# Kernel optimization log

Measured on AMD Instinct MI355X. Metric: run time of the kernel, lower is better.

The kernel has to match this reference:

```python
import jax, jax.numpy as jnp
import numpy as np

D_MODEL = 1024
H = 16
D_K = D_MODEL // H


def setup_inputs() -> dict:
    key = jax.random.key(0)
    ks = jax.random.split(key, 12)
    B, S = 2, 2048
    q = jax.random.normal(ks[0], (B, S, D_MODEL), dtype=jnp.float32)
    k = jax.random.normal(ks[1], (B, S, D_MODEL), dtype=jnp.float32)
    v = jax.random.normal(ks[2], (B, S, D_MODEL), dtype=jnp.float32)
    mask = jax.random.randint(ks[3], (1, 1, S, S), 0, 2, dtype=jnp.int32)
    sc = 1.0 / np.sqrt(D_MODEL)
    wq = jax.random.uniform(ks[4], (D_MODEL, D_MODEL), jnp.float32, -sc, sc)
    bq = jax.random.uniform(ks[5], (D_MODEL,), jnp.float32, -sc, sc)
    wk = jax.random.uniform(ks[6], (D_MODEL, D_MODEL), jnp.float32, -sc, sc)
    bk = jax.random.uniform(ks[7], (D_MODEL,), jnp.float32, -sc, sc)
    wv = jax.random.uniform(ks[8], (D_MODEL, D_MODEL), jnp.float32, -sc, sc)
    bv = jax.random.uniform(ks[9], (D_MODEL,), jnp.float32, -sc, sc)
    wo = jax.random.uniform(ks[10], (D_MODEL, D_MODEL), jnp.float32, -sc, sc)
    bo = jax.random.uniform(ks[11], (D_MODEL,), jnp.float32, -sc, sc)
    return {"q": q, "k": k, "v": v, "mask": mask,
            "wq": wq, "bq": bq, "wk": wk, "bk": bk,
            "wv": wv, "bv": bv, "wo": wo, "bo": bo}


def reference(q, k, v, mask, wq, bq, wk, bk, wv, bv, wo, bo):
    B, S, _ = q.shape
    # linear projections (torch Linear: x @ W.T + b)
    query = q @ wq.T + bq
    key = k @ wk.T + bk
    value = v @ wv.T + bv
    # [B, S, D] -> [B, H, S, d_k]
    query = query.reshape(B, S, H, D_K).transpose(0, 2, 1, 3)
    key = key.reshape(B, S, H, D_K).transpose(0, 2, 1, 3)
    value = value.reshape(B, S, H, D_K).transpose(0, 2, 1, 3)
    scores = jnp.einsum('bhqd,bhkd->bhqk', query, key) / jnp.sqrt(
        jnp.asarray(D_K, query.dtype))
    # NOTE: source uses `-1 ** 9` which is -1 in Python, not -1e9 (soft mask)
    scores = jnp.where(mask == 0, jnp.asarray(-1.0, scores.dtype), scores)
    attn = jax.nn.softmax(scores, axis=-1)
    # source calls dropout(attn) but discards the result -> no-op
    x = jnp.einsum('bhqk,bhkd->bhqd', attn, value)
    x = x.transpose(0, 2, 1, 3).reshape(B, S, H * D_K)
    return x @ wo.T + bo
```

## Files before the change

### kernel.cpp

```cpp
#include <hip/hip_runtime.h>
#include <hip/hip_bf16.h>

#define D_MODEL 1024
#define NH 16
#define DK 64
#define S_LEN 2048
#define BATCH 2
#define M_ROWS (BATCH * S_LEN)

typedef float    floatx4 __attribute__((ext_vector_type(4)));
typedef _Float16 half8   __attribute__((ext_vector_type(8)));
typedef _Float16 half4v  __attribute__((ext_vector_type(4)));

#define LOG2E 1.4426950408889634f

__device__ __forceinline__ half8 ldh8(const _Float16* p) {
    return __builtin_bit_cast(half8, *(const uint4*)p);
}
__device__ __forceinline__ void gld16(const void* g, void* l) {
    __builtin_amdgcn_global_load_lds(
        (const __attribute__((address_space(1))) void*)g,
        (__attribute__((address_space(3))) void*)l, 16, 0, 0);
}
__device__ __forceinline__ float dpp_swap1(float x) {
    return __builtin_bit_cast(float,
        __builtin_amdgcn_mov_dpp(__builtin_bit_cast(int, x), 0xB1, 0xF, 0xF, false));
}

__global__ __launch_bounds__(256)
void cast_h(const float* __restrict__ s0, const float* __restrict__ s1,
            const float* __restrict__ s2, const float* __restrict__ s3,
            _Float16* __restrict__ out, int R) {
    const int z = blockIdx.y;
    const float* src = (z == 0) ? s0 : (z == 1) ? s1 : (z == 2) ? s2 : s3;
    const size_t idx = ((size_t)blockIdx.x * 256 + threadIdx.x) * 4;
    float4 v = *(const float4*)&src[idx];
    half4v h = {(_Float16)v.x, (_Float16)v.y, (_Float16)v.z, (_Float16)v.w};
    *(half4v*)&out[(size_t)z * R * 1024 + idx] = h;
}

template <int OUTMODE>
__global__ __launch_bounds__(256)
void gemm_f16(const _Float16* __restrict__ Abase, const _Float16* __restrict__ Wbase,
              const float* __restrict__ b0, const float* __restrict__ b1,
              const float* __restrict__ b2, void* __restrict__ Obase) {
    __shared__ __align__(16) _Float16 As[128 * 64];
    __shared__ __align__(16) _Float16 Ws[128 * 64];
    const int tid = threadIdx.x;
    const int w = tid >> 6, lane = tid & 63;
    const int l15 = lane & 15, q4 = lane >> 4;
    const int z = (OUTMODE == 1) ? blockIdx.z : 0;
    const int m0 = blockIdx.y * 128, n0 = blockIdx.x * 128;
    const int wm = w >> 1, wn = w & 1;

    const _Float16* A = Abase + (size_t)z * M_ROWS * 1024;
    const _Float16* W = Wbase + (size_t)z * 1024 * 1024;
    const float* bias = (OUTMODE == 1) ? ((z == 0) ? b0 : (z == 1) ? b1 : b2) : b0;

    int srow[4], sseg[4];
#pragma unroll
    for (int i = 0; i < 4; i++) {
        const int slot = i * 256 + tid;
        srow[i] = slot >> 3;
        sseg[i] = ((slot & 7) ^ (srow[i] & 7)) * 8;
    }

    int aoff[4][2], woff[4][2];
#pragma unroll
    for (int r = 0; r < 4; r++) {
        const int ar = wm * 64 + r * 16 + l15;
        const int wr = wn * 64 + r * 16 + l15;
#pragma unroll
        for (int kc = 0; kc < 2; kc++) {
            aoff[r][kc] = (ar * 8 + ((kc * 4 + q4) ^ (ar & 7))) * 8;
            woff[r][kc] = (wr * 8 + ((kc * 4 + q4) ^ (wr & 7))) * 8;
        }
    }

    floatx4 acc[4][4];
#pragma unroll
    for (int r = 0; r < 4; r++)
#pragma unroll
        for (int c = 0; c < 4; c++) acc[r][c] = (floatx4){0.f, 0.f, 0.f, 0.f};

    for (int k0 = 0; k0 < 1024; k0 += 64) {
#pragma unroll
        for (int i = 0; i < 4; i++) {
            const int lb = (i * 256 + w * 64) * 8;
            gld16(&A[(size_t)(m0 + srow[i]) * 1024 + k0 + sseg[i]], &As[lb]);
            gld16(&W[(size_t)(n0 + srow[i]) * 1024 + k0 + sseg[i]], &Ws[lb]);
        }
        __syncthreads();

        half8 af[4][2], wf[4][2];
#pragma unroll
        for (int r = 0; r < 4; r++)
#pragma unroll
            for (int kc = 0; kc < 2; kc++) {
                af[r][kc] = ldh8(&As[aoff[r][kc]]);
                wf[r][kc] = ldh8(&Ws[woff[r][kc]]);
            }
#pragma unroll
        for (int kc = 0; kc < 2; kc++)
#pragma unroll
            for (int r = 0; r < 4; r++)
#pragma unroll
                for (int c = 0; c < 4; c++)
                    acc[r][c] = __builtin_amdgcn_mfma_f32_16x16x32_f16(
                        af[r][kc], wf[c][kc], acc[r][c], 0, 0, 0);
        __syncthreads();
    }

#pragma unroll
    for (int r = 0; r < 4; r++)
#pragma unroll
        for (int c = 0; c < 4; c++)
#pragma unroll
            for (int reg = 0; reg < 4; reg++) {
                const int m = m0 + wm * 64 + r * 16 + q4 * 4 + reg;
                const int n = n0 + wn * 64 + c * 16 + l15;
                float val = acc[r][c][reg] + bias[n];
                if (OUTMODE == 0) {
                    ((float*)Obase)[(size_t)m * 1024 + n] = val;
                } else {
                    if (z == 0) val *= 0.125f * LOG2E;
                    const int b = m >> 11, s = m & 2047;
                    const int h = n >> 6, d = n & 63;
                    _Float16* Oz = (_Float16*)Obase + (size_t)z * M_ROWS * 1024;
                    Oz[(((size_t)(b * 16 + h) * S_LEN + s) << 6) + d] = (_Float16)val;
                }
            }
}

__global__ __launch_bounds__(256)
void vt_trans(const short* __restrict__ Vh, short* __restrict__ Vt) {
    __shared__ __align__(16) short T[64][80];
    const int bh = blockIdx.y;
    const int s0 = blockIdx.x * 64;
    const int t = threadIdx.x;
#pragma unroll
    for (int i = 0; i < 2; i++) {
        const int p = t + i * 256, r = p >> 3, c8 = (p & 7) * 8;
        uint4 raw = *(const uint4*)&Vh[((size_t)bh * S_LEN + s0 + r) * 64 + c8];
        const short* sv = (const short*)&raw;
#pragma unroll
        for (int j = 0; j < 8; j++) T[c8 + j][r] = sv[j];
    }
    __syncthreads();
#pragma unroll
    for (int i = 0; i < 2; i++) {
        const int p = t + i * 256, d = p >> 3, seg = (p & 7) * 8;
        *(uint4*)&Vt[((size_t)bh * DK + d) * S_LEN + s0 + seg] =
            *(const uint4*)&T[d][seg];
    }
}

__global__ __launch_bounds__(256)
void mask_pack(const int* __restrict__ mask, unsigned long long* __restrict__ mb) {
    const int gw = blockIdx.x * 4 + (threadIdx.x >> 6);
    const int lane = threadIdx.x & 63;
    const int row = gw >> 5, wid = gw & 31;
    const int mv = mask[(size_t)row * S_LEN + wid * 64 + lane];
    unsigned long long bal = __ballot(mv != 0);
    if (lane == 0) mb[gw] = bal;
}

__global__ __launch_bounds__(256)
void attn_mfma(const _Float16* __restrict__ Qh, const _Float16* __restrict__ Kh,
               const _Float16* __restrict__ Vt, const unsigned long long* __restrict__ mb,
               _Float16* __restrict__ Xh) {
    __shared__ __align__(16) _Float16 Ks[64 * 64];
    __shared__ __align__(16) _Float16 Vs[64 * 64];
    __shared__ __align__(16) _Float16 Ps[4][32 * 72];

    const int tid = threadIdx.x;
    const int w = tid >> 6, lane = tid & 63;
    const int l15 = lane & 15, q4 = lane >> 4;
    const int bh = blockIdx.y, b = bh >> 4, h = bh & 15;
    const int qb = blockIdx.x * 128 + w * 32;

    const _Float16* Qg = Qh + ((size_t)bh * S_LEN + qb) * DK;
    const _Float16* Kg = Kh + (size_t)bh * S_LEN * DK;
    const _Float16* Vg = Vt + (size_t)bh * DK * S_LEN;

    half8 Aq[2][2];
#pragma unroll
    for (int qs = 0; qs < 2; qs++)
#pragma unroll
        for (int ch = 0; ch < 2; ch++)
            Aq[qs][ch] = ldh8(&Qg[(qs * 16 + l15) * DK + ch * 32 + q4 * 8]);

    int grow[2], gseg[2];
#pragma unroll
    for (int i = 0; i < 2; i++) {
        const int slot = i * 256 + tid;
        grow[i] = slot >> 3;
        gseg[i] = ((slot & 7) ^ (grow[i] & 7)) * 8;
    }

    int foff[4][2];
#pragma unroll
    for (int t4 = 0; t4 < 4; t4++)
#pragma unroll
        for (int ch = 0; ch < 2; ch++)
            foff[t4][ch] = (t4 * 16 + l15) * 64 + (((ch * 4 + q4) ^ (l15 & 7)) * 8);

    int mrow[2][4];
#pragma unroll
    for (int qs = 0; qs < 2; qs++)
#pragma unroll
        for (int reg = 0; reg < 4; reg++)
            mrow[qs][reg] = (qb + qs * 16 + q4 * 4 + reg) * (S_LEN / 64);

    floatx4 O[2][4];
#pragma unroll
    for (int qs = 0; qs < 2; qs++)
#pragma unroll
        for (int nt = 0; nt < 4; nt++) O[qs][nt] = (floatx4){0.f, 0.f, 0.f, 0.f};
    float lsum[2][4] = {{0.f, 0.f, 0.f, 0.f}, {0.f, 0.f, 0.f, 0.f}};

    const bool evenlane = ((lane & 1) == 0);

    for (int j0 = 0; j0 < S_LEN; j0 += 64) {
#pragma unroll
        for (int i = 0; i < 2; i++) {
            const int lb = (i * 256 + w * 64) * 8;
            gld16(&Kg[(size_t)(j0 + grow[i]) * DK + gseg[i]], &Ks[lb]);
            gld16(&Vg[(size_t)grow[i] * S_LEN + j0 + gseg[i]], &Vs[lb]);
        }
        const int jw = j0 >> 6;
        unsigned long long mw[2][4];
#pragma unroll
        for (int qs = 0; qs < 2; qs++)
#pragma unroll
            for (int reg = 0; reg < 4; reg++)
                mw[qs][reg] = mb[mrow[qs][reg] + jw];
        __syncthreads();

        half8 Kf[4][2];
#pragma unroll
        for (int jt = 0; jt < 4; jt++)
#pragma unroll
            for (int ch = 0; ch < 2; ch++)
                Kf[jt][ch] = ldh8(&Ks[foff[jt][ch]]);

#pragma unroll
        for (int qs = 0; qs < 2; qs++) {
            floatx4 Sf[4];
#pragma unroll
            for (int jt = 0; jt < 4; jt++) {
                floatx4 c = (floatx4){0.f, 0.f, 0.f, 0.f};
                c = __builtin_amdgcn_mfma_f32_16x16x32_f16(Aq[qs][0], Kf[jt][0], c, 0, 0, 0);
                c = __builtin_amdgcn_mfma_f32_16x16x32_f16(Aq[qs][1], Kf[jt][1], c, 0, 0, 0);
                Sf[jt] = c;
            }
#pragma unroll
            for (int reg = 0; reg < 4; reg++) {
                const unsigned long long m = mw[qs][reg];
#pragma unroll
                for (int jt = 0; jt < 4; jt++) {
                    float s = Sf[jt][reg];
                    s = ((m >> (jt * 16 + l15)) & 1ull) ? s : -LOG2E;
                    const float p = __builtin_amdgcn_exp2f(s);
                    lsum[qs][reg] += p;
                    const float po = dpp_swap1(p);
                    if (evenlane) {
                        *(unsigned*)&Ps[w][(qs * 16 + q4 * 4 + reg) * 72 +
                                           jt * 16 + l15] =
                            __builtin_bit_cast(unsigned,
                                __builtin_amdgcn_cvt_pkrtz(p, po));
                    }
                }
            }
        }

#pragma unroll
        for (int qs = 0; qs < 2; qs++) {
            half8 Ap[2];
#pragma unroll
            for (int ch = 0; ch < 2; ch++)
                Ap[ch] = ldh8(&Ps[w][(qs * 16 + l15) * 72 + ch * 32 + q4 * 8]);
#pragma unroll
            for (int nt = 0; nt < 4; nt++) {
                O[qs][nt] = __builtin_amdgcn_mfma_f32_16x16x32_f16(
                    Ap[0], ldh8(&Vs[foff[nt][0]]), O[qs][nt], 0, 0, 0);
                O[qs][nt] = __builtin_amdgcn_mfma_f32_16x16x32_f16(
                    Ap[1], ldh8(&Vs[foff[nt][1]]), O[qs][nt], 0, 0, 0);
            }
        }
        __syncthreads();
    }

#pragma unroll
    for (int qs = 0; qs < 2; qs++)
#pragma unroll
        for (int reg = 0; reg < 4; reg++) {
#pragma unroll
            for (int off = 1; off < 16; off <<= 1)
                lsum[qs][reg] += __shfl_xor(lsum[qs][reg], off, 64);
        }
#pragma unroll
    for (int qs = 0; qs < 2; qs++)
#pragma unroll
        for (int reg = 0; reg < 4; reg++) {
            const float inv = 1.0f / lsum[qs][reg];
            const int srow = qb + qs * 16 + q4 * 4 + reg;
            _Float16* Xrow = Xh + (size_t)(b * S_LEN + srow) * 1024 + h * DK;
#pragma unroll
            for (int nt = 0; nt < 4; nt++)
                Xrow[nt * 16 + l15] = (_Float16)(O[qs][nt][reg] * inv);
        }
}

extern "C" void kernel_launch(void* const* d_in, const int* in_sizes, int n_in,
                              void* d_out, int out_size, void* d_ws, size_t ws_size,
                              hipStream_t stream) {
    const float* q  = (const float*)d_in[0];
    const float* k  = (const float*)d_in[1];
    const float* v  = (const float*)d_in[2];
    const int* mask = (const int*)d_in[3];
    const float* wq = (const float*)d_in[4];
    const float* bq = (const float*)d_in[5];
    const float* wk = (const float*)d_in[6];
    const float* bk = (const float*)d_in[7];
    const float* wv = (const float*)d_in[8];
    const float* bv = (const float*)d_in[9];
    const float* wo = (const float*)d_in[10];
    const float* bo = (const float*)d_in[11];
    float* out = (float*)d_out;

    char* ws = (char*)d_ws;
    const size_t MB = 1u << 20;
    _Float16* Wh   = (_Float16*)ws;
    _Float16* Ah   = (_Float16*)(ws + 8 * MB);
    _Float16* QKVh = (_Float16*)(ws + 32 * MB);
    _Float16* Vt   = (_Float16*)(ws + 56 * MB);
    unsigned long long* mb = (unsigned long long*)(ws + 64 * MB);
    _Float16* Xh   = Ah;

    cast_h<<<dim3(1024, 4), 256, 0, stream>>>(wq, wk, wv, wo, Wh, 1024);
    cast_h<<<dim3(4096, 3), 256, 0, stream>>>(q, k, v, nullptr, Ah, M_ROWS);

    gemm_f16<1><<<dim3(8, 32, 3), 256, 0, stream>>>(Ah, Wh, bq, bk, bv, QKVh);

    vt_trans<<<dim3(32, 32), 256, 0, stream>>>(
        (const short*)(QKVh + (size_t)2 * M_ROWS * 1024), (short*)Vt);
    mask_pack<<<S_LEN * (S_LEN / 64) / 4, 256, 0, stream>>>(mask, mb);

    attn_mfma<<<dim3(16, 32), 256, 0, stream>>>(QKVh, QKVh + (size_t)M_ROWS * 1024,
                                                Vt, mb, Xh);

    gemm_f16<0><<<dim3(8, 32, 1), 256, 0, stream>>>(Xh, Wh + (size_t)3 * 1024 * 1024,
                                                    bo, bo, bo, out);
}
```

Baseline: 292.8 us.

## Split attention key range across two blocks and combine partial outputs

The attention kernel's key loop is split in half along a new grid z dimension, doubling the block count. Each half writes unnormalised fp32 partial outputs and row sums to workspace, and a new combine kernel adds them, normalises and writes fp16 X. Row sums are now computed on the matrix cores by multiplying the fp16 probability tile by a ones vector, replacing per-element VALU adds and the final shuffle reduction. The cost is an extra launch plus fp32 partial-output traffic through global memory.

```diff
diff --git a/kernel.cpp b/kernel.cpp
--- a/kernel.cpp
+++ b/kernel.cpp
@@ -168,7 +168,8 @@
 __global__ __launch_bounds__(256)
 void attn_mfma(const _Float16* __restrict__ Qh, const _Float16* __restrict__ Kh,
                const _Float16* __restrict__ Vt, const unsigned long long* __restrict__ mb,
-               _Float16* __restrict__ Xh) {
+               float* __restrict__ O0, float* __restrict__ O1,
+               float* __restrict__ L0, float* __restrict__ L1) {
     __shared__ __align__(16) _Float16 Ks[64 * 64];
     __shared__ __align__(16) _Float16 Vs[64 * 64];
     __shared__ __align__(16) _Float16 Ps[4][32 * 72];
@@ -176,8 +177,13 @@
     const int tid = threadIdx.x;
     const int w = tid >> 6, lane = tid & 63;
     const int l15 = lane & 15, q4 = lane >> 4;
-    const int bh = blockIdx.y, b = bh >> 4, h = bh & 15;
+    const int bh = blockIdx.y;
+    const int z = blockIdx.z;
     const int qb = blockIdx.x * 128 + w * 32;
+    const int jbase = z * (S_LEN / 2);
+
+    float* __restrict__ Op = z ? O1 : O0;
+    float* __restrict__ Lp = z ? L1 : L0;
 
     const _Float16* Qg = Qh + ((size_t)bh * S_LEN + qb) * DK;
     const _Float16* Kg = Kh + (size_t)bh * S_LEN * DK;
@@ -217,11 +223,15 @@
     for (int qs = 0; qs < 2; qs++)
 #pragma unroll
         for (int nt = 0; nt < 4; nt++) O[qs][nt] = (floatx4){0.f, 0.f, 0.f, 0.f};
-    float lsum[2][4] = {{0.f, 0.f, 0.f, 0.f}, {0.f, 0.f, 0.f, 0.f}};
-
+    floatx4 lacc[2];
+    lacc[0] = (floatx4){0.f, 0.f, 0.f, 0.f};
+    lacc[1] = (floatx4){0.f, 0.f, 0.f, 0.f};
+
+    const half8 ones8 = {(_Float16)1.f, (_Float16)1.f, (_Float16)1.f, (_Float16)1.f,
+                         (_Float16)1.f, (_Float16)1.f, (_Float16)1.f, (_Float16)1.f};
     const bool evenlane = ((lane & 1) == 0);
 
-    for (int j0 = 0; j0 < S_LEN; j0 += 64) {
+    for (int j0 = jbase; j0 < jbase + S_LEN / 2; j0 += 64) {
 #pragma unroll
         for (int i = 0; i < 2; i++) {
             const int lb = (i * 256 + w * 64) * 8;
@@ -262,7 +272,6 @@
                     float s = Sf[jt][reg];
                     s = ((m >> (jt * 16 + l15)) & 1ull) ? s : -LOG2E;
                     const float p = __builtin_amdgcn_exp2f(s);
-                    lsum[qs][reg] += p;
                     const float po = dpp_swap1(p);
                     if (evenlane) {
                         *(unsigned*)&Ps[w][(qs * 16 + q4 * 4 + reg) * 72 +
@@ -280,6 +289,8 @@
 #pragma unroll
             for (int ch = 0; ch < 2; ch++)
                 Ap[ch] = ldh8(&Ps[w][(qs * 16 + l15) * 72 + ch * 32 + q4 * 8]);
+            lacc[qs] = __builtin_amdgcn_mfma_f32_16x16x32_f16(Ap[0], ones8, lacc[qs], 0, 0, 0);
+            lacc[qs] = __builtin_amdgcn_mfma_f32_16x16x32_f16(Ap[1], ones8, lacc[qs], 0, 0, 0);
 #pragma unroll
             for (int nt = 0; nt < 4; nt++) {
                 O[qs][nt] = __builtin_amdgcn_mfma_f32_16x16x32_f16(
@@ -292,24 +303,34 @@
     }
 
 #pragma unroll
-    for (int qs = 0; qs < 2; qs++)
+    for (int qs = 0; qs < 2; qs++) {
 #pragma unroll
         for (int reg = 0; reg < 4; reg++) {
-#pragma unroll
-            for (int off = 1; off < 16; off <<= 1)
-                lsum[qs][reg] += __shfl_xor(lsum[qs][reg], off, 64);
-        }
-#pragma unroll
-    for (int qs = 0; qs < 2; qs++)
-#pragma unroll
-        for (int reg = 0; reg < 4; reg++) {
-            const float inv = 1.0f / lsum[qs][reg];
-            const int srow = qb + qs * 16 + q4 * 4 + reg;
-            _Float16* Xrow = Xh + (size_t)(b * S_LEN + srow) * 1024 + h * DK;
+            const int row = qb + qs * 16 + q4 * 4 + reg;
+            float* Orow = Op + ((size_t)bh * S_LEN + row) * DK;
 #pragma unroll
             for (int nt = 0; nt < 4; nt++)
-                Xrow[nt * 16 + l15] = (_Float16)(O[qs][nt][reg] * inv);
-        }
+                Orow[nt * 16 + l15] = O[qs][nt][reg];
+            if (l15 == 0)
+                Lp[(size_t)bh * S_LEN + row] = lacc[qs][reg];
+        }
+    }
+}
+
+__global__ __launch_bounds__(256)
+void combine_o(const float* __restrict__ O0, const float* __restrict__ O1,
+               const float* __restrict__ L0, const float* __restrict__ L1,
+               _Float16* __restrict__ Xh) {
+    const int g = blockIdx.x * 256 + threadIdx.x;
+    const int orow = g >> 4, d4 = (g & 15) << 2;
+    const int bh = orow >> 11, s = orow & 2047;
+    const int b = bh >> 4, h = bh & 15;
+    const float4 a = *(const float4*)&O0[(size_t)orow * DK + d4];
+    const float4 c = *(const float4*)&O1[(size_t)orow * DK + d4];
+    const float inv = 1.0f / (L0[orow] + L1[orow]);
+    half4v o = {(_Float16)((a.x + c.x) * inv), (_Float16)((a.y + c.y) * inv),
+                (_Float16)((a.z + c.z) * inv), (_Float16)((a.w + c.w) * inv)};
+    *(half4v*)&Xh[((size_t)(b * S_LEN + s)) * 1024 + h * DK + d4] = o;
 }
 
 extern "C" void kernel_launch(void* const* d_in, const int* in_sizes, int n_in,
@@ -336,7 +357,11 @@
     _Float16* QKVh = (_Float16*)(ws + 32 * MB);
     _Float16* Vt   = (_Float16*)(ws + 56 * MB);
     unsigned long long* mb = (unsigned long long*)(ws + 64 * MB);
-    _Float16* Xh   = Ah;
+    float* Lp0 = (float*)(ws + 65 * MB);
+    float* Lp1 = (float*)(ws + 65 * MB + 512 * 1024);
+    _Float16* Xh = Ah;
+    float* Op0 = (float*)(ws + 16 * MB);
+    float* Op1 = (float*)(ws + 66 * MB);
 
     cast_h<<<dim3(1024, 4), 256, 0, stream>>>(wq, wk, wv, wo, Wh, 1024);
     cast_h<<<dim3(4096, 3), 256, 0, stream>>>(q, k, v, nullptr, Ah, M_ROWS);
@@ -347,8 +372,10 @@
         (const short*)(QKVh + (size_t)2 * M_ROWS * 1024), (short*)Vt);
     mask_pack<<<S_LEN * (S_LEN / 64) / 4, 256, 0, stream>>>(mask, mb);
 
-    attn_mfma<<<dim3(16, 32), 256, 0, stream>>>(QKVh, QKVh + (size_t)M_ROWS * 1024,
-                                                Vt, mb, Xh);
+    attn_mfma<<<dim3(16, 32, 2), 256, 0, stream>>>(
+        QKVh, QKVh + (size_t)M_ROWS * 1024, Vt, mb, Op0, Op1, Lp0, Lp1);
+
+    combine_o<<<4096, 256, 0, stream>>>(Op0, Op1, Lp0, Lp1, Xh);
 
     gemm_f16<0><<<dim3(8, 32, 1), 256, 0, stream>>>(Xh, Wh + (size_t)3 * 1024 * 1024,
                                                     bo, bo, bo, out);
```

Measured after the change: 304.2 us. 1.04x slower.
